# Kernel optimization log

Hardware: AMD Instinct MI355X
Metric: run time of the kernel (lower is better)

Reference implementation:

```python
import jax, jax.numpy as jnp
import numpy as np

B, G, T, N = 4, 8, 30, 60
CT, CN = 1, 60
FD, IDD = 256, 256
E = FD + IDD          # 512
H = 8                 # (FD+IDD)//head_dim
L = 6                 # num_layers
VP1 = 51              # num_id_vocabulary + 1
PE = 32               # rel_pe_length
DFF = 4 * E


def _ln(x, g, b, eps=1e-5):
    m = x.mean(-1, keepdims=True)
    v = ((x - m) ** 2).mean(-1, keepdims=True)
    return (x - m) / jnp.sqrt(v + eps) * g + b


def _mha(qx, kx, vx, Wqkv, bqkv, Wo, bo, bias, h):
    # torch nn.MultiheadAttention with add_zero_attn=True; bias is additive
    # attn bias of shape [B, h, Lq, Lk+1] (already padded for the zero-attn col).
    e = qx.shape[-1]
    d = e // h
    Wq, Wk, Wv = jnp.split(Wqkv, 3, axis=0)
    bq, bk, bv = jnp.split(bqkv, 3)
    q = qx @ Wq.T + bq
    k = kx @ Wk.T + bk
    v = vx @ Wv.T + bv
    b_, lq, _ = q.shape
    lk = k.shape[1]
    z = jnp.zeros((b_, 1, e), q.dtype)
    k = jnp.concatenate([k, z], axis=1)   # add_zero_attn appends zero key
    v = jnp.concatenate([v, z], axis=1)
    qh = q.reshape(b_, lq, h, d).transpose(0, 2, 1, 3)
    kh = k.reshape(b_, lk + 1, h, d).transpose(0, 2, 1, 3)
    vh = v.reshape(b_, lk + 1, h, d).transpose(0, 2, 1, 3)
    s = jnp.einsum('bhqd,bhkd->bhqk', qh, kh) / jnp.sqrt(jnp.float32(d)) + bias
    p = jax.nn.softmax(s, axis=-1)
    o = jnp.einsum('bhqk,bhkd->bhqd', p, vh).transpose(0, 2, 1, 3).reshape(b_, lq, e)
    return o @ Wo.T + bo


def _forward(tf, uf, ids, tt_, ut_, tm, um, Ww, Wout, rpe,
             saW, sab, saO, saob, sag, sabn,
             caW, cab, caO, caob, cag, cabn,
             f1, fb1, f2, fb2, fg, fbn):
    b, g, t, n, fd = tf.shape
    _, _, ct, cn, _ = uf.shape
    id_dim = Ww.shape[0]
    e = fd + id_dim
    nl = caW.shape[0]
    h = rpe.shape[-1]
    pe = rpe.shape[1]
    # one_hot(label) @ W_word.T == W_word[:, label]
    traj_id = Ww.T[ids]                                        # b g t n id
    unk_id = jnp.broadcast_to(Ww[:, VP1 - 1], (b, g, ct, cn, id_dim))
    traj = jnp.concatenate([tf, traj_id], -1).reshape(b * g, t * n, e)
    unk = jnp.concatenate([uf, unk_id], -1)                    # b g ct cn e

    tt = tt_.reshape(b * g, t * n)
    ut = ut_.reshape(b * g, ct * cn)
    neg = jnp.float32(-jnp.inf)
    zero = jnp.float32(0)
    causal = jnp.where(tt[:, None, :] >= ut[:, :, None], neg, zero)  # bg q k
    kpm = jnp.where(tm.reshape(b * g, t * n), neg, zero)             # bg k
    # torch rel_pos_map[u, t] = u - t; negative torch indices wrap -> mod pe
    rel_idx = (ut[:, :, None] - tt[:, None, :]) % pe                 # bg q k
    sa_bias = jnp.pad(
        jnp.where(um.reshape(b * g * ct, cn), neg, zero)[:, None, None, :],
        ((0, 0), (0, 0), (0, 0), (0, 1)))

    for l in range(nl):
        if l > 0:
            x = unk.reshape(b * g * ct, cn, e)
            y = _mha(x, x, x, saW[l - 1], sab[l - 1], saO[l - 1], saob[l - 1], sa_bias, h)
            unk = _ln(x + y, sag[l - 1], sabn[l - 1]).reshape(b, g, ct, cn, e)
        q = unk.reshape(b * g, ct * cn, e)
        rel = rpe[l][rel_idx]                                  # bg q k h  (gathered rel-PE)
        bias = causal[:, None] + jnp.transpose(rel, (0, 3, 1, 2)) + kpm[:, None, None, :]
        bias = jnp.pad(bias, ((0, 0), (0, 0), (0, 0), (0, 1)))
        y = _mha(q, traj, traj, caW[l], cab[l], caO[l], caob[l], bias, h)
        x = _ln(q + y, cag[l], cabn[l])
        hh = jax.nn.gelu(x @ f1[l].T + fb1[l], approximate=False) @ f2[l].T + fb2[l]
        x = _ln(x + hh, fg[l], fbn[l])
        unk = x.reshape(b, g, ct, cn, e)
    # final layer logits (eval mode): shared embed_to_word head, no bias
    return unk[..., fd:] @ Wout.T


def setup_inputs():
    key = jax.random.key(0)
    ks = iter(jax.random.split(key, 48))
    nrm = lambda shape, s=0.02: jax.random.normal(next(ks), shape, jnp.float32) * s
    return {
        'trajectory_features': jax.random.normal(next(ks), (B, G, T, N, FD), jnp.float32),
        'unknown_features': jax.random.normal(next(ks), (B, G, CT, CN, FD), jnp.float32),
        'trajectory_id_labels': jax.random.randint(next(ks), (B, G, T, N), 0, VP1),
        'trajectory_times': jax.random.randint(next(ks), (B, G, T, N), 0, PE),
        'unknown_times': jax.random.randint(next(ks), (B, G, CT, CN), 0, PE),
        'trajectory_masks': jnp.zeros((B, G, T, N), bool),
        'unknown_masks': jnp.zeros((B, G, CT, CN), bool),
        'use_decoder_checkpoint': 0,
        'W_word': nrm((IDD, VP1), 0.05),
        'W_out': nrm((VP1, IDD), 0.05),
        'rel_pos_embeds': nrm((L, PE, H), 0.1),
        'sa_Wqkv': nrm((L - 1, 3 * E, E)), 'sa_bqkv': jnp.zeros((L - 1, 3 * E)),
        'sa_Wo': nrm((L - 1, E, E)), 'sa_bo': jnp.zeros((L - 1, E)),
        'sa_ln_g': jnp.ones((L - 1, E)), 'sa_ln_b': jnp.zeros((L - 1, E)),
        'ca_Wqkv': nrm((L, 3 * E, E)), 'ca_bqkv': jnp.zeros((L, 3 * E)),
        'ca_Wo': nrm((L, E, E)), 'ca_bo': jnp.zeros((L, E)),
        'ca_ln_g': jnp.ones((L, E)), 'ca_ln_b': jnp.zeros((L, E)),
        'ffn_W1': nrm((L, DFF, E)), 'ffn_b1': jnp.zeros((L, DFF)),
        'ffn_W2': nrm((L, E, DFF)), 'ffn_b2': jnp.zeros((L, E)),
        'ffn_ln_g': jnp.ones((L, E)), 'ffn_ln_b': jnp.zeros((L, E)),
    }


def reference(trajectory_features, unknown_features, trajectory_id_labels,
              trajectory_times, unknown_times, trajectory_masks, unknown_masks,
              use_decoder_checkpoint, W_word, W_out, rel_pos_embeds,
              sa_Wqkv, sa_bqkv, sa_Wo, sa_bo, sa_ln_g, sa_ln_b,
              ca_Wqkv, ca_bqkv, ca_Wo, ca_bo, ca_ln_g, ca_ln_b,
              ffn_W1, ffn_b1, ffn_W2, ffn_b2, ffn_ln_g, ffn_ln_b):
    return _forward(trajectory_features, unknown_features, trajectory_id_labels,
                    trajectory_times, unknown_times, trajectory_masks, unknown_masks,
                    W_word, W_out, rel_pos_embeds,
                    sa_Wqkv, sa_bqkv, sa_Wo, sa_bo, sa_ln_g, sa_ln_b,
                    ca_Wqkv, ca_bqkv, ca_Wo, ca_bo, ca_ln_g, ca_ln_b,
                    ffn_W1, ffn_b1, ffn_W2, ffn_b2, ffn_ln_g, ffn_ln_b)
```

## Files before the change

kernel.cpp:

```cpp
#include <hip/hip_runtime.h>
#include <cmath>

__device__ __forceinline__ float bflo(unsigned int u) {
  union { unsigned int i; float f; } v; v.i = u << 16; return v.f;
}
__device__ __forceinline__ float bfhi(unsigned int u) {
  union { unsigned int i; float f; } v; v.i = u & 0xffff0000u; return v.f;
}
__device__ __forceinline__ float bf2f(unsigned short u) {
  union { unsigned int i; float f; } v; v.i = ((unsigned int)u) << 16; return v.f;
}
__device__ __forceinline__ unsigned short f2bf(float f) {
  union { float f; unsigned int i; } v; v.f = f;
  unsigned int i = v.i;
  return (unsigned short)((i + 0x7fffu + ((i >> 16) & 1u)) >> 16);
}
__device__ __forceinline__ unsigned int pack2bf(float a, float b) {
  return (unsigned int)f2bf(a) | ((unsigned int)f2bf(b) << 16);
}

typedef __attribute__((ext_vector_type(8))) short short8;
typedef __attribute__((ext_vector_type(4))) float floatx4;

__global__ __launch_bounds__(256) void conv_kernel(
    const float* __restrict__ in, unsigned short* __restrict__ out, int n)
{
  int i = (blockIdx.x * 256 + threadIdx.x) << 2;
  if (i >= n) return;
  float4 v = *reinterpret_cast<const float4*>(in + i);
  ushort4 o;
  o.x = f2bf(v.x); o.y = f2bf(v.y); o.z = f2bf(v.z); o.w = f2bf(v.w);
  *reinterpret_cast<ushort4*>(out + i) = o;
}

__global__ __launch_bounds__(256) void build_wwt_kernel(
    const float* __restrict__ Ww, unsigned short* __restrict__ Wwt)
{
  int c = blockIdx.x;
  int r = threadIdx.x;
  Wwt[c * 256 + r] = f2bf(Ww[r * 51 + c]);
}

__global__ __launch_bounds__(512, 2) void gemm256(
    const unsigned short* __restrict__ A,
    const unsigned short* __restrict__ W,
    const float* __restrict__ bias,
    unsigned short* __restrict__ C)
{
  __shared__ __align__(16) unsigned short LA[2][2][8192];
  __shared__ __align__(16) unsigned short LB[2][2][8192];
  const int tid = threadIdx.x;
  const int wave = tid >> 6, lane = tid & 63;
  const int quad = lane >> 4, mrow = lane & 15;
  const int wm = wave >> 2, wn = wave & 3;
  const size_t ldK = 512;
  const int nt = 8;

  int f = blockIdx.x;
  {
    const int nwg = gridDim.x;
    const int q = nwg >> 3, r = nwg & 7;
    const int x = f & 7, i = f >> 3;
    f = (x < r ? x * (q + 1) : r * (q + 1) + (x - r) * q) + i;
  }
  const int bn = (f & 3) << 8;
  const int bm = (f >> 2) << 8;

  floatx4 acc[8][4];
#pragma unroll
  for (int i = 0; i < 8; ++i)
#pragma unroll
    for (int j = 0; j < 4; ++j) acc[i][j] = (floatx4){0.f, 0.f, 0.f, 0.f};

  const int srow0 = (wave << 4) + (lane >> 2);
  const int srow1 = srow0 + 128;
  const int sslot = (lane & 3) ^ ((srow0 >> 1) & 3);

#define STAGEH(dst, srcbase, rowoff, kelem)                                          \
  do {                                                                               \
    __builtin_amdgcn_global_load_lds(                                                \
        (const __attribute__((address_space(1))) unsigned int*)(                     \
            (srcbase) + (size_t)((rowoff) + srow0) * ldK + (kelem) + sslot * 8),     \
        (__attribute__((address_space(3))) unsigned int*)((dst) + wave * 512),       \
        16, 0, 0);                                                                   \
    __builtin_amdgcn_global_load_lds(                                                \
        (const __attribute__((address_space(1))) unsigned int*)(                     \
            (srcbase) + (size_t)((rowoff) + srow1) * ldK + (kelem) + sslot * 8),     \
        (__attribute__((address_space(3))) unsigned int*)((dst) + 4096 + wave * 512),\
        16, 0, 0);                                                                   \
  } while (0)

  STAGEH(&LB[0][0][0], W, bn, 0);
  STAGEH(&LA[0][0][0], A, bm, 0);
  STAGEH(&LB[0][1][0], W, bn, 32);
  STAGEH(&LA[0][1][0], A, bm, 32);
  STAGEH(&LB[1][0][0], W, bn, 64);
  STAGEH(&LA[1][0][0], A, bm, 64);
  STAGEH(&LB[1][1][0], W, bn, 96);
  asm volatile("s_waitcnt vmcnt(6)" ::: "memory");
  __builtin_amdgcn_s_barrier();

  const int rsw = ((quad ^ ((mrow >> 1) & 3)) << 3);
  const int arowb = wm * 128 + mrow;
  const int brows = wn * 64 + mrow;

  for (int T = 0; T < nt; ++T) {
    const int c = T & 1;
    unsigned short* A0 = &LA[c][0][0];
    unsigned short* A1 = &LA[c][1][0];
    unsigned short* B0 = &LB[c][0][0];
    unsigned short* B1 = &LB[c][1][0];
    short8 afr[4], bfr[4];

#pragma unroll
    for (int i = 0; i < 4; ++i)
      afr[i] = *reinterpret_cast<const short8*>(A0 + (arowb + i * 16) * 32 + rsw);
#pragma unroll
    for (int j = 0; j < 4; ++j)
      bfr[j] = *reinterpret_cast<const short8*>(B0 + (brows + j * 16) * 32 + rsw);
    if (T + 1 < nt) STAGEH(&LA[c ^ 1][1][0], A, bm, (T + 1) * 64 + 32);
    __builtin_amdgcn_s_barrier();
    asm volatile("s_waitcnt lgkmcnt(0)" ::: "memory");
    __builtin_amdgcn_s_setprio(1);
#pragma unroll
    for (int i = 0; i < 4; ++i)
#pragma unroll
      for (int j = 0; j < 4; ++j)
        acc[i][j] = __builtin_amdgcn_mfma_f32_16x16x32_bf16(afr[i], bfr[j], acc[i][j], 0, 0, 0);
    __builtin_amdgcn_s_setprio(0);
    __builtin_amdgcn_s_barrier();

#pragma unroll
    for (int i = 0; i < 4; ++i)
      afr[i] = *reinterpret_cast<const short8*>(A0 + (arowb + (i + 4) * 16) * 32 + rsw);
    if (T + 2 < nt) STAGEH(&LB[c][0][0], W, bn, (T + 2) * 64);
    __builtin_amdgcn_s_barrier();
    asm volatile("s_waitcnt lgkmcnt(0)" ::: "memory");
    __builtin_amdgcn_s_setprio(1);
#pragma unroll
    for (int i = 0; i < 4; ++i)
#pragma unroll
      for (int j = 0; j < 4; ++j)
        acc[i + 4][j] = __builtin_amdgcn_mfma_f32_16x16x32_bf16(afr[i], bfr[j], acc[i + 4][j], 0, 0, 0);
    __builtin_amdgcn_s_setprio(0);
    __builtin_amdgcn_s_barrier();

#pragma unroll
    for (int i = 0; i < 4; ++i)
      afr[i] = *reinterpret_cast<const short8*>(A1 + (arowb + i * 16) * 32 + rsw);
#pragma unroll
    for (int j = 0; j < 4; ++j)
      bfr[j] = *reinterpret_cast<const short8*>(B1 + (brows + j * 16) * 32 + rsw);
    if (T + 2 < nt) STAGEH(&LA[c][0][0], A, bm, (T + 2) * 64);
    __builtin_amdgcn_s_barrier();
    asm volatile("s_waitcnt lgkmcnt(0)" ::: "memory");
    __builtin_amdgcn_s_setprio(1);
#pragma unroll
    for (int i = 0; i < 4; ++i)
#pragma unroll
      for (int j = 0; j < 4; ++j)
        acc[i][j] = __builtin_amdgcn_mfma_f32_16x16x32_bf16(afr[i], bfr[j], acc[i][j], 0, 0, 0);
    __builtin_amdgcn_s_setprio(0);
    __builtin_amdgcn_s_barrier();

#pragma unroll
    for (int i = 0; i < 4; ++i)
      afr[i] = *reinterpret_cast<const short8*>(A1 + (arowb + (i + 4) * 16) * 32 + rsw);
    if (T + 2 < nt) STAGEH(&LB[c][1][0], W, bn, (T + 2) * 64 + 32);
    __builtin_amdgcn_s_barrier();
    asm volatile("s_waitcnt lgkmcnt(0)" ::: "memory");
    __builtin_amdgcn_s_setprio(1);
#pragma unroll
    for (int i = 0; i < 4; ++i)
#pragma unroll
      for (int j = 0; j < 4; ++j)
        acc[i + 4][j] = __builtin_amdgcn_mfma_f32_16x16x32_bf16(afr[i], bfr[j], acc[i + 4][j], 0, 0, 0);
    __builtin_amdgcn_s_setprio(0);
    if (T + 2 < nt)
      asm volatile("s_waitcnt vmcnt(6)" ::: "memory");
    else
      asm volatile("s_waitcnt vmcnt(0)" ::: "memory");
    __builtin_amdgcn_s_barrier();
  }
#undef STAGEH

  const int col0 = lane & 15;
  const int row0 = (lane >> 4) << 2;
#pragma unroll
  for (int i = 0; i < 8; ++i)
#pragma unroll
    for (int j = 0; j < 4; ++j) {
      int col = bn + wn * 64 + j * 16 + col0;
      float bv = bias[col];
#pragma unroll
      for (int r = 0; r < 4; ++r) {
        int row = bm + wm * 128 + i * 16 + row0 + r;
        C[(size_t)row * 1024 + col] = f2bf(acc[i][j][r] + bv);
      }
    }
}

__global__ __launch_bounds__(256) void gemm_mfma(
    const unsigned short* __restrict__ A, int lda,
    const unsigned short* __restrict__ W, int ldw,
    const float* __restrict__ bias,
    void* __restrict__ Cv, int ldc,
    int K, int act, int cbf16, int swz)
{
  __shared__ __align__(16) unsigned short As[2][128 * 32];
  __shared__ __align__(16) unsigned short Bs[2][128 * 32];
  const int tid = threadIdx.x;
  const int wave = tid >> 6, lane = tid & 63;

  int bxi = blockIdx.x, byi = blockIdx.y;
  if (swz) {
    int f = byi * gridDim.x + bxi;
    int q = (gridDim.x * gridDim.y) >> 3;
    f = (f & 7) * q + (f >> 3);
    bxi = f % gridDim.x;
    byi = f / gridDim.x;
  }
  const int bm = byi * 128, bn = bxi * 128;
  const int wm = (wave >> 1) << 6, wn = (wave & 1) << 6;

  floatx4 acc[4][4];
#pragma unroll
  for (int i = 0; i < 4; ++i)
#pragma unroll
    for (int j = 0; j < 4; ++j) acc[i][j] = (floatx4){0.f, 0.f, 0.f, 0.f};

  const int srow = (wave << 5) + (lane >> 2);
  const int chsw = (lane & 3) ^ ((srow >> 1) & 3);
  const int scol = chsw << 3;
  const unsigned short* Ag  = A + (size_t)(bm + srow) * lda + scol;
  const unsigned short* Wg  = W + (size_t)(bn + srow) * ldw + scol;
  const unsigned short* Ag2 = Ag + (size_t)16 * lda;
  const unsigned short* Wg2 = Wg + (size_t)16 * ldw;
  const int ldsw = (wave << 5) * 32;

  const int arow = lane & 15;
  const int rsw  = (arow >> 1) & 3;
  const int chrd = (lane >> 4) ^ rsw;
  const int aoff = (wm + arow) * 32 + (chrd << 3);
  const int boff = (wn + arow) * 32 + (chrd << 3);

  const int nt = K >> 5;

#define STAGE(b, t)                                                                 \
  do {                                                                              \
    const int k0_ = (t) << 5;                                                       \
    __builtin_amdgcn_global_load_lds(                                               \
        (const __attribute__((address_space(1))) unsigned int*)(Ag + k0_),          \
        (__attribute__((address_space(3))) unsigned int*)(As[(b)] + ldsw), 16, 0, 0); \
    __builtin_amdgcn_global_load_lds(                                               \
        (const __attribute__((address_space(1))) unsigned int*)(Ag2 + k0_),         \
        (__attribute__((address_space(3))) unsigned int*)(As[(b)] + ldsw + 16 * 32), 16, 0, 0); \
    __builtin_amdgcn_global_load_lds(                                               \
        (const __attribute__((address_space(1))) unsigned int*)(Wg + k0_),          \
        (__attribute__((address_space(3))) unsigned int*)(Bs[(b)] + ldsw), 16, 0, 0); \
    __builtin_amdgcn_global_load_lds(                                               \
        (const __attribute__((address_space(1))) unsigned int*)(Wg2 + k0_),         \
        (__attribute__((address_space(3))) unsigned int*)(Bs[(b)] + ldsw + 16 * 32), 16, 0, 0); \
  } while (0)

  STAGE(0, 0);
  if (nt > 1) STAGE(1, 1);

  int cur = 0;
  for (int t = 0; t < nt; ++t) {
    if (t + 1 < nt) asm volatile("s_waitcnt vmcnt(4)\n\ts_barrier" ::: "memory");
    else            asm volatile("s_waitcnt vmcnt(0)\n\ts_barrier" ::: "memory");

    short8 af[4], bf[4];
#pragma unroll
    for (int i = 0; i < 4; ++i) {
      af[i] = *reinterpret_cast<const short8*>(&As[cur][aoff + (i << 4) * 32]);
      bf[i] = *reinterpret_cast<const short8*>(&Bs[cur][boff + (i << 4) * 32]);
    }
    asm volatile("s_waitcnt lgkmcnt(0)\n\ts_barrier" ::: "memory");
    if (t + 2 < nt) STAGE(cur, t + 2);

#pragma unroll
    for (int i = 0; i < 4; ++i)
#pragma unroll
      for (int j = 0; j < 4; ++j)
        acc[i][j] = __builtin_amdgcn_mfma_f32_16x16x32_bf16(af[i], bf[j], acc[i][j], 0, 0, 0);
    cur ^= 1;
  }
#undef STAGE

  const int col0 = lane & 15;
  const int row0 = (lane >> 4) << 2;
#pragma unroll
  for (int i = 0; i < 4; ++i) {
#pragma unroll
    for (int j = 0; j < 4; ++j) {
      int col = bn + wn + (j << 4) + col0;
      float bv = bias ? bias[col] : 0.f;
#pragma unroll
      for (int r = 0; r < 4; ++r) {
        int row = bm + wm + (i << 4) + row0 + r;
        float v = acc[i][j][r] + bv;
        if (act) v = 0.5f * v * (1.f + erff(v * 0.70710678f));
        if (cbf16) ((unsigned short*)Cv)[(size_t)row * ldc + col] = f2bf(v);
        else       ((float*)Cv)[(size_t)row * ldc + col] = v;
      }
    }
  }
}

__device__ __forceinline__ float wred_max(float v) {
#pragma unroll
  for (int off = 32; off > 0; off >>= 1) v = fmaxf(v, __shfl_xor(v, off, 64));
  return v;
}
__device__ __forceinline__ float wred_sum(float v) {
#pragma unroll
  for (int off = 32; off > 0; off >>= 1) v += __shfl_xor(v, off, 64);
  return v;
}

#define LDK 72
__global__ __launch_bounds__(512) void attn_mfma_kernel(
    const unsigned short* __restrict__ Qp,
    const unsigned short* __restrict__ KVb,
    unsigned short* __restrict__ O,
    const int* __restrict__ tt, const int* __restrict__ ut,
    const unsigned char* __restrict__ km,
    const float* __restrict__ rel)
{
  const int bg = blockIdx.x >> 3, h = blockIdx.x & 7;
  const int tid = threadIdx.x;
  const int grp = tid >> 8;
  const int wave = (tid >> 6) & 3;
  const int lane = tid & 63;
  const int quad = lane >> 4, mrow = lane & 15;

  __shared__ __align__(16) unsigned short SMEM[6 * 64 * LDK];
  unsigned short* Ks = SMEM + grp * (3 * 64 * LDK);
  unsigned short* Vt = Ks + 64 * LDK;
  unsigned short* Ps = Vt + 64 * LDK;

  const int qa = wave * 16 + mrow;
  const int qc = qa < 60 ? qa : 59;
  const unsigned short* qptr = Qp + (size_t)(bg * 60 + qc) * 512 + h * 64 + quad * 8;
  const short8 af0 = *reinterpret_cast<const short8*>(qptr);
  const short8 af1 = *reinterpret_cast<const short8*>(qptr + 32);

  const float relreg = rel[(lane & 31) * 8 + h];

  int tq[4];
  float m[4], l[4];
  floatx4 acc[4];
#pragma unroll
  for (int r = 0; r < 4; ++r) {
    int qo = wave * 16 + quad * 4 + r;
    tq[r] = ut[bg * 60 + (qo < 60 ? qo : 59)];
    m[r] = grp ? -1e30f : 0.f;
    l[r] = grp ? 0.f : 1.f;
  }
#pragma unroll
  for (int nt = 0; nt < 4; ++nt) acc[nt] = (floatx4){0.f, 0.f, 0.f, 0.f};

  const int sk = tid & 255;
  const int stok = sk >> 2, schk = sk & 3;

  for (int it = 0; it < 15; ++it) {
    const int k0 = (grp + 2 * it) << 6;
    __syncthreads();
    {
      const int key = k0 + stok;
      uint4 kr0 = {0,0,0,0}, kr1 = {0,0,0,0}, vr0 = {0,0,0,0}, vr1 = {0,0,0,0};
      if (key < 1800) {
        const unsigned short* kb = KVb + ((size_t)bg * 1800 + key) * 1024 + h * 64 + schk * 16;
        kr0 = *reinterpret_cast<const uint4*>(kb);
        kr1 = *reinterpret_cast<const uint4*>(kb + 8);
        vr0 = *reinterpret_cast<const uint4*>(kb + 512);
        vr1 = *reinterpret_cast<const uint4*>(kb + 520);
      }
      *reinterpret_cast<uint4*>(&Ks[stok * LDK + schk * 16]) = kr0;
      *reinterpret_cast<uint4*>(&Ks[stok * LDK + schk * 16 + 8]) = kr1;
      unsigned int wv[8] = {vr0.x, vr0.y, vr0.z, vr0.w, vr1.x, vr1.y, vr1.z, vr1.w};
#pragma unroll
      for (int e = 0; e < 16; ++e)
        Vt[(schk * 16 + e) * LDK + stok] = (unsigned short)(wv[e >> 1] >> ((e & 1) * 16));
    }
    int meta = 0x10000;
    {
      int kk = k0 + lane;
      if (kk < 1800) {
        int base = bg * 1800 + kk;
        meta = tt[base] | (km[base] ? 0x10000 : 0);
      }
    }
    __syncthreads();

    floatx4 S[4];
#pragma unroll
    for (int nt = 0; nt < 4; ++nt) {
      const unsigned short* kb = Ks + (nt * 16 + mrow) * LDK + quad * 8;
      short8 b0 = *reinterpret_cast<const short8*>(kb);
      short8 b1 = *reinterpret_cast<const short8*>(kb + 32);
      floatx4 s = (floatx4){0.f, 0.f, 0.f, 0.f};
      s = __builtin_amdgcn_mfma_f32_16x16x32_bf16(af0, b0, s, 0, 0, 0);
      s = __builtin_amdgcn_mfma_f32_16x16x32_bf16(af1, b1, s, 0, 0, 0);
      S[nt] = s;
    }
    int mcol[4];
#pragma unroll
    for (int nt = 0; nt < 4; ++nt)
      mcol[nt] = __builtin_amdgcn_ds_bpermute((nt * 16 + mrow) << 2, meta);
    float sv[4][4];
#pragma unroll
    for (int nt = 0; nt < 4; ++nt) {
      int tk = mcol[nt] & 0xffff;
      int bad0 = mcol[nt] >> 16;
#pragma unroll
      for (int r = 0; r < 4; ++r) {
        float v = S[nt][r] * 0.125f;
        int ridx = (tq[r] - tk) & 31;
        v += __int_as_float(__builtin_amdgcn_ds_bpermute(ridx << 2, __float_as_int(relreg)));
        sv[nt][r] = (bad0 | (tk >= tq[r])) ? -1e30f : v;
      }
    }
#pragma unroll
    for (int r = 0; r < 4; ++r) {
      float rm = fmaxf(fmaxf(sv[0][r], sv[1][r]), fmaxf(sv[2][r], sv[3][r]));
#pragma unroll
      for (int d = 1; d < 16; d <<= 1) rm = fmaxf(rm, __shfl_xor(rm, d, 64));
      float nm = fmaxf(m[r], rm);
      float corr = __expf(m[r] - nm);
      float ps = 0.f;
      const int prow = (wave * 16 + quad * 4 + r) * LDK + mrow;
#pragma unroll
      for (int nt = 0; nt < 4; ++nt) {
        float p = __expf(sv[nt][r] - nm);
        ps += p;
        Ps[prow + nt * 16] = f2bf(p);
      }
#pragma unroll
      for (int d = 1; d < 16; d <<= 1) ps += __shfl_xor(ps, d, 64);
      l[r] = l[r] * corr + ps;
      m[r] = nm;
#pragma unroll
      for (int nt = 0; nt < 4; ++nt) acc[nt][r] *= corr;
    }
    const unsigned short* pp = Ps + (wave * 16 + mrow) * LDK + quad * 8;
    short8 a0 = *reinterpret_cast<const short8*>(pp);
    short8 a1 = *reinterpret_cast<const short8*>(pp + 32);
#pragma unroll
    for (int nt = 0; nt < 4; ++nt) {
      const unsigned short* vb = Vt + (nt * 16 + mrow) * LDK + quad * 8;
      short8 b0 = *reinterpret_cast<const short8*>(vb);
      short8 b1 = *reinterpret_cast<const short8*>(vb + 32);
      acc[nt] = __builtin_amdgcn_mfma_f32_16x16x32_bf16(a0, b0, acc[nt], 0, 0, 0);
      acc[nt] = __builtin_amdgcn_mfma_f32_16x16x32_bf16(a1, b1, acc[nt], 0, 0, 0);
    }
  }

  __syncthreads();
  float* MA = (float*)SMEM;
  float* Ml = (float*)(SMEM + 64 * 68 * 2);
  float* Ll = Ml + 64;
  if (grp == 1) {
#pragma unroll
    for (int r = 0; r < 4; ++r) {
      int row = wave * 16 + quad * 4 + r;
#pragma unroll
      for (int nt = 0; nt < 4; ++nt)
        MA[row * 68 + nt * 16 + mrow] = acc[nt][r];
      if (mrow == 0) { Ml[row] = m[r]; Ll[row] = l[r]; }
    }
  }
  __syncthreads();
  if (grp == 0) {
#pragma unroll
    for (int r = 0; r < 4; ++r) {
      int row = wave * 16 + quad * 4 + r;
      float m1 = Ml[row], l1 = Ll[row];
      float M = fmaxf(m[r], m1);
      float c0 = __expf(m[r] - M), c1 = __expf(m1 - M);
      float invL = 1.f / (l[r] * c0 + l1 * c1);
      if (row < 60) {
        unsigned short* op = O + (size_t)(bg * 60 + row) * 512 + h * 64;
#pragma unroll
        for (int nt = 0; nt < 4; ++nt) {
          float o = (acc[nt][r] * c0 + MA[row * 68 + nt * 16 + mrow] * c1) * invL;
          op[nt * 16 + mrow] = f2bf(o);
        }
      }
    }
  }
}

#define QPB 32
#define QPW 8
__global__ __launch_bounds__(256) void attn2_kernel(
    const unsigned short* __restrict__ Qp, int qs,
    const unsigned short* __restrict__ Kp, int ks,
    const unsigned short* __restrict__ Vp, int vs,
    unsigned short* __restrict__ O, int os, int kLen,
    const unsigned char* __restrict__ kmask)
{
  const int bg = blockIdx.x >> 3;
  const int h  = blockIdx.x & 7;
  const int q0 = blockIdx.y * QPB;
  const int tid = threadIdx.x;
  const int wave = tid >> 6, lane = tid & 63;

  __shared__ float Qs[QPB][68];
  __shared__ float Ks[64][68];
  __shared__ float Vs[64][68];
  __shared__ float Ps[QPB][68];

  {
    int qr = tid >> 3, j = tid & 7;
    int q = q0 + qr;
    float f[8] = {0, 0, 0, 0, 0, 0, 0, 0};
    if (q < 60) {
      uint4 v = *reinterpret_cast<const uint4*>(Qp + (size_t)(bg * 60 + q) * qs + h * 64 + j * 8);
      f[0] = bflo(v.x); f[1] = bfhi(v.x); f[2] = bflo(v.y); f[3] = bfhi(v.y);
      f[4] = bflo(v.z); f[5] = bfhi(v.z); f[6] = bflo(v.w); f[7] = bfhi(v.w);
    }
#pragma unroll
    for (int e = 0; e < 8; ++e) Qs[qr][j * 8 + e] = f[e];
  }

  float m[QPW], l[QPW], acc[QPW];
#pragma unroll
  for (int i = 0; i < QPW; ++i) { m[i] = 0.f; l[i] = 1.f; acc[i] = 0.f; }

  const int std = tid >> 2;
  const int stj = tid & 3;

  for (int k0 = 0; k0 < kLen; k0 += 64) {
    __syncthreads();
    const bool sok = (k0 + std) < kLen;
    {
      const unsigned short* kb = Kp + ((size_t)bg * kLen + k0 + std) * ks + h * 64 + stj * 16;
      float f[16];
#pragma unroll
      for (int e = 0; e < 16; ++e) f[e] = 0.f;
      if (sok) {
        uint4 v0 = *reinterpret_cast<const uint4*>(kb);
        uint4 v1 = *reinterpret_cast<const uint4*>(kb + 8);
        f[0] = bflo(v0.x); f[1] = bfhi(v0.x); f[2]  = bflo(v0.y); f[3]  = bfhi(v0.y);
        f[4] = bflo(v0.z); f[5] = bfhi(v0.z); f[6]  = bflo(v0.w); f[7]  = bfhi(v0.w);
        f[8] = bflo(v1.x); f[9] = bfhi(v1.x); f[10] = bflo(v1.y); f[11] = bfhi(v1.y);
        f[12] = bflo(v1.z); f[13] = bfhi(v1.z); f[14] = bflo(v1.w); f[15] = bfhi(v1.w);
      }
#pragma unroll
      for (int e = 0; e < 16; ++e) Ks[stj * 16 + e][std] = f[e];
    }
    {
      const unsigned short* vb = Vp + ((size_t)bg * kLen + k0 + std) * vs + h * 64;
#pragma unroll
      for (int c = 0; c < 2; ++c) {
        int off = c * 32 + stj * 8;
        float f[8] = {0, 0, 0, 0, 0, 0, 0, 0};
        if (sok) {
          uint4 v = *reinterpret_cast<const uint4*>(vb + off);
          f[0] = bflo(v.x); f[1] = bfhi(v.x); f[2] = bflo(v.y); f[3] = bfhi(v.y);
          f[4] = bflo(v.z); f[5] = bfhi(v.z); f[6] = bflo(v.w); f[7] = bfhi(v.w);
        }
#pragma unroll
        for (int e = 0; e < 8; ++e) Vs[std][off + e] = f[e];
      }
    }
    const int kk = k0 + lane;
    const bool kok = kk < kLen;
    unsigned char kmv = 0;
    if (kok && kmask) kmv = kmask[(size_t)bg * kLen + kk];
    __syncthreads();

    float s[QPW];
#pragma unroll
    for (int i = 0; i < QPW; ++i) s[i] = 0.f;
    for (int d = 0; d < 64; ++d) {
      float kv = Ks[d][lane];
#pragma unroll
      for (int i = 0; i < QPW; ++i)
        s[i] = fmaf(Qs[wave * QPW + i][d], kv, s[i]);
    }

    const int kmax = min(64, kLen - k0);
#pragma unroll
    for (int i = 0; i < QPW; ++i) {
      float svv = s[i] * 0.125f;
      if (kmv || !kok) svv = -1e30f;
      float nm = fmaxf(m[i], wred_max(svv));
      float p = __expf(svv - nm);
      float ts = wred_sum(p);
      float corr = __expf(m[i] - nm);
      l[i] = l[i] * corr + ts;
      acc[i] *= corr;
      m[i] = nm;
      Ps[wave * QPW + i][lane] = p;
    }
    for (int k = 0; k < kmax; ++k) {
      float v = Vs[k][lane];
#pragma unroll
      for (int i = 0; i < QPW; ++i)
        acc[i] = fmaf(Ps[wave * QPW + i][k], v, acc[i]);
    }
  }

#pragma unroll
  for (int i = 0; i < QPW; ++i) {
    int q = q0 + wave * QPW + i;
    if (q < 60)
      O[(size_t)(bg * 60 + q) * os + h * 64 + lane] = f2bf(acc[i] / l[i]);
  }
}

__global__ __launch_bounds__(256) void add_ln_kernel(
    const float* __restrict__ a, const float* __restrict__ b,
    const float* __restrict__ g, const float* __restrict__ be,
    float* __restrict__ o, unsigned short* __restrict__ ob)
{
  const int t = blockIdx.x;
  const int tid = threadIdx.x;
  const int wave = tid >> 6, lane = tid & 63;
  const size_t base = (size_t)t * 512;
  float v0 = a[base + tid] + b[base + tid];
  float v1 = a[base + 256 + tid] + b[base + 256 + tid];
  __shared__ float red[4];
  float s = wred_sum(v0 + v1);
  if (lane == 0) red[wave] = s;
  __syncthreads();
  float mean = (red[0] + red[1] + red[2] + red[3]) * (1.0f / 512.0f);
  float d0 = v0 - mean, d1 = v1 - mean;
  float vs = wred_sum(d0 * d0 + d1 * d1);
  __syncthreads();
  if (lane == 0) red[wave] = vs;
  __syncthreads();
  float var = (red[0] + red[1] + red[2] + red[3]) * (1.0f / 512.0f);
  float rstd = rsqrtf(var + 1e-5f);
  float r0 = d0 * rstd * g[tid] + be[tid];
  float r1 = d1 * rstd * g[256 + tid] + be[256 + tid];
  o[base + tid] = r0;
  o[base + 256 + tid] = r1;
  ob[base + tid] = f2bf(r0);
  ob[base + 256 + tid] = f2bf(r1);
}

__global__ __launch_bounds__(256) void build_traj_kernel(
    const float* __restrict__ tf, const int* __restrict__ ids,
    const unsigned short* __restrict__ Wwt, unsigned short* __restrict__ traj)
{
  int idx = blockIdx.x * 256 + threadIdx.x;
  int tok = idx >> 6;
  int sub = idx & 63;
  uint4 o;
  if (sub < 32) {
    const float* ip = tf + ((size_t)tok << 8) + sub * 8;
    float4 a = *reinterpret_cast<const float4*>(ip);
    float4 b = *reinterpret_cast<const float4*>(ip + 4);
    o.x = pack2bf(a.x, a.y); o.y = pack2bf(a.z, a.w);
    o.z = pack2bf(b.x, b.y); o.w = pack2bf(b.z, b.w);
  } else {
    int id = ids[tok];
    o = *reinterpret_cast<const uint4*>(Wwt + id * 256 + (sub - 32) * 8);
  }
  *reinterpret_cast<uint4*>(traj + ((size_t)tok << 9) + sub * 8) = o;
}

__global__ __launch_bounds__(256) void build_unk_kernel(
    const float* __restrict__ uf, const float* __restrict__ Ww,
    float* __restrict__ x, unsigned short* __restrict__ xb)
{
  int idx = blockIdx.x * 256 + threadIdx.x;
  int tok = idx >> 6;
  int sub = idx & 63;
  float f[8];
  if (sub < 32) {
    const float* ip = uf + ((size_t)tok << 8) + sub * 8;
    float4 a = *reinterpret_cast<const float4*>(ip);
    float4 b = *reinterpret_cast<const float4*>(ip + 4);
    f[0] = a.x; f[1] = a.y; f[2] = a.z; f[3] = a.w;
    f[4] = b.x; f[5] = b.y; f[6] = b.z; f[7] = b.w;
  } else {
    const float* wp = Ww + (size_t)((sub - 32) * 8) * 51 + 50;
#pragma unroll
    for (int e = 0; e < 8; ++e) f[e] = wp[e * 51];
  }
  size_t base = ((size_t)tok << 9) + sub * 8;
  float4 x0 = {f[0], f[1], f[2], f[3]};
  float4 x1 = {f[4], f[5], f[6], f[7]};
  *reinterpret_cast<float4*>(x + base) = x0;
  *reinterpret_cast<float4*>(x + base + 4) = x1;
  uint4 o;
  o.x = pack2bf(f[0], f[1]); o.y = pack2bf(f[2], f[3]);
  o.z = pack2bf(f[4], f[5]); o.w = pack2bf(f[6], f[7]);
  *reinterpret_cast<uint4*>(xb + base) = o;
}

__global__ __launch_bounds__(64) void head_kernel(
    const float* __restrict__ x, const float* __restrict__ Wout, float* __restrict__ out)
{
  const int t = blockIdx.x;
  const int tid = threadIdx.x;
  __shared__ float xs[256];
  for (int i = tid; i < 256; i += 64) xs[i] = x[(size_t)t * 512 + 256 + i];
  __syncthreads();
  if (tid < 51) {
    const float* w = Wout + tid * 256;
    float s = 0.f;
    for (int k = 0; k < 256; ++k) s = fmaf(xs[k], w[k], s);
    out[t * 51 + tid] = s;
  }
}

extern "C" void kernel_launch(void* const* d_in, const int* in_sizes, int n_in,
                              void* d_out, int out_size, void* d_ws, size_t ws_size,
                              hipStream_t stream) {
  const float* tf  = (const float*)d_in[0];
  const float* uf  = (const float*)d_in[1];
  const int*   ids = (const int*)d_in[2];
  const int*   tt  = (const int*)d_in[3];
  const int*   ut  = (const int*)d_in[4];
  const unsigned char* tm = (const unsigned char*)d_in[5];
  const unsigned char* um = (const unsigned char*)d_in[6];
  const float* Ww   = (const float*)d_in[8];
  const float* Wout = (const float*)d_in[9];
  const float* rpe  = (const float*)d_in[10];
  const float* saW  = (const float*)d_in[11];
  const float* sab  = (const float*)d_in[12];
  const float* saO  = (const float*)d_in[13];
  const float* saob = (const float*)d_in[14];
  const float* sag  = (const float*)d_in[15];
  const float* sabn = (const float*)d_in[16];
  const float* caW  = (const float*)d_in[17];
  const float* cab  = (const float*)d_in[18];
  const float* caO  = (const float*)d_in[19];
  const float* caob = (const float*)d_in[20];
  const float* cag  = (const float*)d_in[21];
  const float* cabn = (const float*)d_in[22];
  const float* f1   = (const float*)d_in[23];
  const float* fb1  = (const float*)d_in[24];
  const float* f2   = (const float*)d_in[25];
  const float* fb2  = (const float*)d_in[26];
  const float* fg   = (const float*)d_in[27];
  const float* fbn  = (const float*)d_in[28];

  unsigned short* trajb = (unsigned short*)d_ws;
  unsigned short* KVb   = trajb + (size_t)29491200;
  unsigned short* qkvb  = KVb   + (size_t)58982400;
  unsigned short* hb    = qkvb  + (size_t)2949120;
  unsigned short* xb    = hb    + (size_t)3932160;
  float* x    = (float*)(xb + (size_t)983040);
  float* ybuf = x + (size_t)983040;
  unsigned short* wtail = (unsigned short*)(ybuf + (size_t)983040);

  const size_t NEED = (size_t)200540160 + (size_t)24117248 * 2 + 32768;
  const bool pre = ws_size >= NEED;
  unsigned short* wsa  = wtail;
  unsigned short* wsaO = wsa  + (size_t)3932160;
  unsigned short* wca  = wsaO + (size_t)1310720;
  unsigned short* wcaO = wca  + (size_t)4718592;
  unsigned short* wf1  = wcaO + (size_t)1572864;
  unsigned short* wf2  = wf1  + (size_t)6291456;
  unsigned short* Wwt  = wf2  + (size_t)6291456;
  unsigned short* wconv = wtail;
  unsigned short* WwtF  = wconv + (size_t)1048576;

  if (pre) {
    conv_kernel<<<dim3(3840), dim3(256), 0, stream>>>(saW, wsa, 3932160);
    conv_kernel<<<dim3(1280), dim3(256), 0, stream>>>(saO, wsaO, 1310720);
    conv_kernel<<<dim3(4608), dim3(256), 0, stream>>>(caW, wca, 4718592);
    conv_kernel<<<dim3(1536), dim3(256), 0, stream>>>(caO, wcaO, 1572864);
    conv_kernel<<<dim3(6144), dim3(256), 0, stream>>>(f1, wf1, 6291456);
    conv_kernel<<<dim3(6144), dim3(256), 0, stream>>>(f2, wf2, 6291456);
  }
  unsigned short* wwt = pre ? Wwt : WwtF;
  build_wwt_kernel<<<dim3(51), dim3(256), 0, stream>>>(Ww, wwt);

  build_traj_kernel<<<dim3(14400), dim3(256), 0, stream>>>(tf, ids, wwt, trajb);
  build_unk_kernel<<<dim3(480), dim3(256), 0, stream>>>(uf, Ww, x, xb);

  for (int l = 0; l < 6; ++l) {
    if (l > 0) {
      int sl = l - 1;
      const unsigned short* wq;
      if (pre) wq = wsa + (size_t)sl * 786432;
      else {
        conv_kernel<<<dim3(768), dim3(256), 0, stream>>>(saW + (size_t)sl * 786432, wconv, 786432);
        wq = wconv;
      }
      gemm_mfma<<<dim3(12, 15), dim3(256), 0, stream>>>(
          xb, 512, wq, 512, sab + sl * 1536, qkvb, 1536, 512, 0, 1, 0);
      attn2_kernel<<<dim3(256, 2), dim3(256), 0, stream>>>(
          qkvb, 1536, qkvb + 512, 1536, qkvb + 1024, 1536, hb, 512, 60, um);
      const unsigned short* wo;
      if (pre) wo = wsaO + (size_t)sl * 262144;
      else {
        conv_kernel<<<dim3(256), dim3(256), 0, stream>>>(saO + (size_t)sl * 262144, wconv, 262144);
        wo = wconv;
      }
      gemm_mfma<<<dim3(4, 15), dim3(256), 0, stream>>>(
          hb, 512, wo, 512, saob + sl * 512, ybuf, 512, 512, 0, 0, 0);
      add_ln_kernel<<<dim3(1920), dim3(256), 0, stream>>>(x, ybuf, sag + sl * 512, sabn + sl * 512, x, xb);
    }
    const unsigned short* wqkv;
    if (pre) wqkv = wca + (size_t)l * 786432;
    else {
      conv_kernel<<<dim3(768), dim3(256), 0, stream>>>(caW + (size_t)l * 786432, wconv, 786432);
      wqkv = wconv;
    }
    gemm256<<<dim3(900), dim3(512), 0, stream>>>(
        trajb, wqkv + 262144, cab + l * 1536 + 512, KVb);
    gemm_mfma<<<dim3(4, 15), dim3(256), 0, stream>>>(
        xb, 512, wqkv, 512, cab + l * 1536, qkvb, 512, 512, 0, 1, 0);
    attn_mfma_kernel<<<dim3(256), dim3(512), 0, stream>>>(
        qkvb, KVb, hb, tt, ut, tm, rpe + l * 256);
    const unsigned short* wco;
    if (pre) wco = wcaO + (size_t)l * 262144;
    else {
      conv_kernel<<<dim3(256), dim3(256), 0, stream>>>(caO + (size_t)l * 262144, wconv, 262144);
      wco = wconv;
    }
    gemm_mfma<<<dim3(4, 15), dim3(256), 0, stream>>>(
        hb, 512, wco, 512, caob + l * 512, ybuf, 512, 512, 0, 0, 0);
    add_ln_kernel<<<dim3(1920), dim3(256), 0, stream>>>(x, ybuf, cag + l * 512, cabn + l * 512, x, xb);
    const unsigned short* w1;
    if (pre) w1 = wf1 + (size_t)l * 1048576;
    else {
      conv_kernel<<<dim3(1024), dim3(256), 0, stream>>>(f1 + (size_t)l * 1048576, wconv, 1048576);
      w1 = wconv;
    }
    gemm_mfma<<<dim3(16, 15), dim3(256), 0, stream>>>(
        xb, 512, w1, 512, fb1 + l * 2048, hb, 2048, 512, 1, 1, 0);
    const unsigned short* w2;
    if (pre) w2 = wf2 + (size_t)l * 1048576;
    else {
      conv_kernel<<<dim3(1024), dim3(256), 0, stream>>>(f2 + (size_t)l * 1048576, wconv, 1048576);
      w2 = wconv;
    }
    gemm_mfma<<<dim3(4, 15), dim3(256), 0, stream>>>(
        hb, 2048, w2, 2048, fb2 + l * 512, ybuf, 512, 2048, 0, 0, 0);
    add_ln_kernel<<<dim3(1920), dim3(256), 0, stream>>>(x, ybuf, fg + l * 512, fbn + l * 512, x, xb);
  }
  head_kernel<<<dim3(1920), dim3(64), 0, stream>>>(x, Wout, (float*)d_out);
}
```

Measured before the change: 1.908 ms.

## Shrink cross-attention KV GEMM tile to 128x256 with single-K-step double buffering

Reworks the K/V projection GEMM to use 128-row M tiles instead of 256, with a 32-wide K step and a simpler two-stage LDS ring. Fewer accumulators and less LDS per block allow launch bounds of 4 blocks per CU, and the grid doubles to 1800. The intent is higher occupancy and a better fill of the GPU's compute units. The cost is less data reuse per tile, more global reloads of W, more barriers per unit of work, and a simplified block remap that assumes the grid divides by 8.

```diff
diff --git a/kernel.cpp b/kernel.cpp
--- a/kernel.cpp
+++ b/kernel.cpp
@@ -41,86 +41,78 @@
   Wwt[c * 256 + r] = f2bf(Ww[r * 51 + c]);
 }
 
-__global__ __launch_bounds__(512, 2) void gemm256(
+__global__ __launch_bounds__(512, 4) void gemm256(
     const unsigned short* __restrict__ A,
     const unsigned short* __restrict__ W,
     const float* __restrict__ bias,
     unsigned short* __restrict__ C)
 {
-  __shared__ __align__(16) unsigned short LA[2][2][8192];
-  __shared__ __align__(16) unsigned short LB[2][2][8192];
+  __shared__ __align__(16) unsigned short LA[2][4096];
+  __shared__ __align__(16) unsigned short LB[2][8192];
   const int tid = threadIdx.x;
   const int wave = tid >> 6, lane = tid & 63;
   const int quad = lane >> 4, mrow = lane & 15;
   const int wm = wave >> 2, wn = wave & 3;
   const size_t ldK = 512;
-  const int nt = 8;
+  const int nt = 16;
 
   int f = blockIdx.x;
   {
-    const int nwg = gridDim.x;
-    const int q = nwg >> 3, r = nwg & 7;
-    const int x = f & 7, i = f >> 3;
-    f = (x < r ? x * (q + 1) : r * (q + 1) + (x - r) * q) + i;
+    const int q = gridDim.x >> 3;
+    f = (f & 7) * q + (f >> 3);
   }
   const int bn = (f & 3) << 8;
-  const int bm = (f >> 2) << 8;
-
-  floatx4 acc[8][4];
-#pragma unroll
-  for (int i = 0; i < 8; ++i)
+  const int bm = (f >> 2) << 7;
+
+  floatx4 acc[4][4];
+#pragma unroll
+  for (int i = 0; i < 4; ++i)
 #pragma unroll
     for (int j = 0; j < 4; ++j) acc[i][j] = (floatx4){0.f, 0.f, 0.f, 0.f};
 
-  const int srow0 = (wave << 4) + (lane >> 2);
-  const int srow1 = srow0 + 128;
-  const int sslot = (lane & 3) ^ ((srow0 >> 1) & 3);
-
-#define STAGEH(dst, srcbase, rowoff, kelem)                                          \
+  const int srow = tid >> 2;
+  const int sslot = (tid & 3) ^ ((srow >> 1) & 3);
+
+#define STAGE32(p, kelem)                                                            \
   do {                                                                               \
     __builtin_amdgcn_global_load_lds(                                                \
         (const __attribute__((address_space(1))) unsigned int*)(                     \
-            (srcbase) + (size_t)((rowoff) + srow0) * ldK + (kelem) + sslot * 8),     \
-        (__attribute__((address_space(3))) unsigned int*)((dst) + wave * 512),       \
+            A + (size_t)(bm + srow) * ldK + (kelem) + sslot * 8),                    \
+        (__attribute__((address_space(3))) unsigned int*)(&LA[(p)][0] + wave * 512), \
         16, 0, 0);                                                                   \
     __builtin_amdgcn_global_load_lds(                                                \
         (const __attribute__((address_space(1))) unsigned int*)(                     \
-            (srcbase) + (size_t)((rowoff) + srow1) * ldK + (kelem) + sslot * 8),     \
-        (__attribute__((address_space(3))) unsigned int*)((dst) + 4096 + wave * 512),\
+            W + (size_t)(bn + srow) * ldK + (kelem) + sslot * 8),                    \
+        (__attribute__((address_space(3))) unsigned int*)(&LB[(p)][0] + wave * 512), \
+        16, 0, 0);                                                                   \
+    __builtin_amdgcn_global_load_lds(                                                \
+        (const __attribute__((address_space(1))) unsigned int*)(                     \
+            W + (size_t)(bn + 128 + srow) * ldK + (kelem) + sslot * 8),              \
+        (__attribute__((address_space(3))) unsigned int*)(&LB[(p)][4096] + wave * 512), \
         16, 0, 0);                                                                   \
   } while (0)
 
-  STAGEH(&LB[0][0][0], W, bn, 0);
-  STAGEH(&LA[0][0][0], A, bm, 0);
-  STAGEH(&LB[0][1][0], W, bn, 32);
-  STAGEH(&LA[0][1][0], A, bm, 32);
-  STAGEH(&LB[1][0][0], W, bn, 64);
-  STAGEH(&LA[1][0][0], A, bm, 64);
-  STAGEH(&LB[1][1][0], W, bn, 96);
-  asm volatile("s_waitcnt vmcnt(6)" ::: "memory");
+  STAGE32(0, 0);
+  STAGE32(1, 32);
+  asm volatile("s_waitcnt vmcnt(3)" ::: "memory");
   __builtin_amdgcn_s_barrier();
 
   const int rsw = ((quad ^ ((mrow >> 1) & 3)) << 3);
-  const int arowb = wm * 128 + mrow;
+  const int arowb = wm * 64 + mrow;
   const int brows = wn * 64 + mrow;
 
   for (int T = 0; T < nt; ++T) {
-    const int c = T & 1;
-    unsigned short* A0 = &LA[c][0][0];
-    unsigned short* A1 = &LA[c][1][0];
-    unsigned short* B0 = &LB[c][0][0];
-    unsigned short* B1 = &LB[c][1][0];
+    const int p = T & 1;
     short8 afr[4], bfr[4];
-
 #pragma unroll
     for (int i = 0; i < 4; ++i)
-      afr[i] = *reinterpret_cast<const short8*>(A0 + (arowb + i * 16) * 32 + rsw);
+      afr[i] = *reinterpret_cast<const short8*>(&LA[p][(arowb + i * 16) * 32 + rsw]);
 #pragma unroll
     for (int j = 0; j < 4; ++j)
-      bfr[j] = *reinterpret_cast<const short8*>(B0 + (brows + j * 16) * 32 + rsw);
-    if (T + 1 < nt) STAGEH(&LA[c ^ 1][1][0], A, bm, (T + 1) * 64 + 32);
+      bfr[j] = *reinterpret_cast<const short8*>(&LB[p][(brows + j * 16) * 32 + rsw]);
+    asm volatile("s_waitcnt lgkmcnt(0)" ::: "memory");
     __builtin_amdgcn_s_barrier();
-    asm volatile("s_waitcnt lgkmcnt(0)" ::: "memory");
+    if (T + 2 < nt) STAGE32(p, (T + 2) * 32);
     __builtin_amdgcn_s_setprio(1);
 #pragma unroll
     for (int i = 0; i < 4; ++i)
@@ -128,73 +120,23 @@
       for (int j = 0; j < 4; ++j)
         acc[i][j] = __builtin_amdgcn_mfma_f32_16x16x32_bf16(afr[i], bfr[j], acc[i][j], 0, 0, 0);
     __builtin_amdgcn_s_setprio(0);
+    if (T + 2 < nt) asm volatile("s_waitcnt vmcnt(3)" ::: "memory");
+    else            asm volatile("s_waitcnt vmcnt(0)" ::: "memory");
     __builtin_amdgcn_s_barrier();
-
-#pragma unroll
-    for (int i = 0; i < 4; ++i)
-      afr[i] = *reinterpret_cast<const short8*>(A0 + (arowb + (i + 4) * 16) * 32 + rsw);
-    if (T + 2 < nt) STAGEH(&LB[c][0][0], W, bn, (T + 2) * 64);
-    __builtin_amdgcn_s_barrier();
-    asm volatile("s_waitcnt lgkmcnt(0)" ::: "memory");
-    __builtin_amdgcn_s_setprio(1);
-#pragma unroll
-    for (int i = 0; i < 4; ++i)
-#pragma unroll
-      for (int j = 0; j < 4; ++j)
-        acc[i + 4][j] = __builtin_amdgcn_mfma_f32_16x16x32_bf16(afr[i], bfr[j], acc[i + 4][j], 0, 0, 0);
-    __builtin_amdgcn_s_setprio(0);
-    __builtin_amdgcn_s_barrier();
-
-#pragma unroll
-    for (int i = 0; i < 4; ++i)
-      afr[i] = *reinterpret_cast<const short8*>(A1 + (arowb + i * 16) * 32 + rsw);
-#pragma unroll
-    for (int j = 0; j < 4; ++j)
-      bfr[j] = *reinterpret_cast<const short8*>(B1 + (brows + j * 16) * 32 + rsw);
-    if (T + 2 < nt) STAGEH(&LA[c][0][0], A, bm, (T + 2) * 64);
-    __builtin_amdgcn_s_barrier();
-    asm volatile("s_waitcnt lgkmcnt(0)" ::: "memory");
-    __builtin_amdgcn_s_setprio(1);
-#pragma unroll
-    for (int i = 0; i < 4; ++i)
-#pragma unroll
-      for (int j = 0; j < 4; ++j)
-        acc[i][j] = __builtin_amdgcn_mfma_f32_16x16x32_bf16(afr[i], bfr[j], acc[i][j], 0, 0, 0);
-    __builtin_amdgcn_s_setprio(0);
-    __builtin_amdgcn_s_barrier();
-
-#pragma unroll
-    for (int i = 0; i < 4; ++i)
-      afr[i] = *reinterpret_cast<const short8*>(A1 + (arowb + (i + 4) * 16) * 32 + rsw);
-    if (T + 2 < nt) STAGEH(&LB[c][1][0], W, bn, (T + 2) * 64 + 32);
-    __builtin_amdgcn_s_barrier();
-    asm volatile("s_waitcnt lgkmcnt(0)" ::: "memory");
-    __builtin_amdgcn_s_setprio(1);
-#pragma unroll
-    for (int i = 0; i < 4; ++i)
-#pragma unroll
-      for (int j = 0; j < 4; ++j)
-        acc[i + 4][j] = __builtin_amdgcn_mfma_f32_16x16x32_bf16(afr[i], bfr[j], acc[i + 4][j], 0, 0, 0);
-    __builtin_amdgcn_s_setprio(0);
-    if (T + 2 < nt)
-      asm volatile("s_waitcnt vmcnt(6)" ::: "memory");
-    else
-      asm volatile("s_waitcnt vmcnt(0)" ::: "memory");
-    __builtin_amdgcn_s_barrier();
-  }
-#undef STAGEH
+  }
+#undef STAGE32
 
   const int col0 = lane & 15;
   const int row0 = (lane >> 4) << 2;
 #pragma unroll
-  for (int i = 0; i < 8; ++i)
+  for (int i = 0; i < 4; ++i)
 #pragma unroll
     for (int j = 0; j < 4; ++j) {
       int col = bn + wn * 64 + j * 16 + col0;
       float bv = bias[col];
 #pragma unroll
       for (int r = 0; r < 4; ++r) {
-        int row = bm + wm * 128 + i * 16 + row0 + r;
+        int row = bm + wm * 64 + i * 16 + row0 + r;
         C[(size_t)row * 1024 + col] = f2bf(acc[i][j][r] + bv);
       }
     }
@@ -807,7 +749,7 @@
       conv_kernel<<<dim3(768), dim3(256), 0, stream>>>(caW + (size_t)l * 786432, wconv, 786432);
       wqkv = wconv;
     }
-    gemm256<<<dim3(900), dim3(512), 0, stream>>>(
+    gemm256<<<dim3(1800), dim3(512), 0, stream>>>(
         trajb, wqkv + 262144, cab + l * 1536 + 512, KVb);
     gemm_mfma<<<dim3(4, 15), dim3(256), 0, stream>>>(
         xb, 512, wqkv, 512, cab + l * 1536, qkvb, 512, 512, 0, 1, 0);
```

Measured after the change: 1.822 ms, median of 2. 1.05x faster.
